# Optimization experiments

Measured on AMD Instinct MI355X. Metric: run time of the kernel, lower is better.

## Reference

```python
import jax, jax.numpy as jnp
import numpy as np

N = 32768   # points
C = 64      # channels (in == out, required by residual)
K = 16      # nsample
SP = 8      # share_planes
S = C // SP # attention channels per group
E = N * K


def _bn(t, g, b, eps=1e-5):
    # torch BatchNorm1d training-mode forward: biased batch variance
    m = t.mean(0)
    v = t.var(0)
    return (t - m) * jax.lax.rsqrt(v + eps) * g + b


def setup_inputs() -> dict:
    rng = np.random.default_rng(0)
    pos = (rng.standard_normal((N, 3)) * 10.0).astype(np.float32)
    # kNN graph (loop=True -> self is among the K nearest, distance 0), chunked
    sq = (pos ** 2).sum(1)
    nbr = np.empty((N, K), dtype=np.int64)
    chunk = 2048
    for s0 in range(0, N, chunk):
        s1 = min(s0 + chunk, N)
        d = sq[s0:s1, None] + sq[None, :] - 2.0 * (pos[s0:s1] @ pos.T)
        nbr[s0:s1] = np.argpartition(d, K - 1, axis=1)[:, :K]
    # PyG convention: edge_index[0]=source j (neighbor), edge_index[1]=target i
    edge_index = np.stack([nbr.reshape(-1),
                           np.repeat(np.arange(N, dtype=np.int64), K)])

    def lin_w(fo, fi):
        b = 1.0 / np.sqrt(fi)
        return jnp.asarray(rng.uniform(-b, b, size=(fo, fi)).astype(np.float32))

    def lin_b(fo, fi):
        b = 1.0 / np.sqrt(fi)
        return jnp.asarray(rng.uniform(-b, b, size=(fo,)).astype(np.float32))

    ones = lambda n: jnp.ones((n,), jnp.float32)
    zeros = lambda n: jnp.zeros((n,), jnp.float32)

    return {
        'pos': jnp.asarray(pos),
        'x': jnp.asarray(rng.standard_normal((N, C)).astype(np.float32)),
        'W1': lin_w(C, C),
        'Wk': lin_w(C, C), 'bk': lin_b(C, C),
        'Wq': lin_w(C, C), 'bq': lin_b(C, C),
        'Wv': lin_w(C, C), 'bv': lin_b(C, C),
        'p1_w': lin_w(3, 3), 'p1_b': lin_b(3, 3),
        'p_bn_g': ones(3), 'p_bn_b': zeros(3),
        'p2_w': lin_w(C, 3), 'p2_b': lin_b(C, 3),
        'w_bn1_g': ones(C), 'w_bn1_b': zeros(C),
        'w1_w': lin_w(S, C), 'w1_b': lin_b(S, C),
        'w_bn2_g': ones(S), 'w_bn2_b': zeros(S),
        'w2_w': lin_w(S, S), 'w2_b': lin_b(S, S),
        'W3': lin_w(C, C),
        'bn1_g': ones(C), 'bn1_b': zeros(C),
        'bn2_g': ones(C), 'bn2_b': zeros(C),
        'bn3_g': ones(C), 'bn3_b': zeros(C),
        'edge_index': jnp.asarray(edge_index),
    }


def reference(pos, x, W1, Wk, bk, Wq, bq, Wv, bv,
              p1_w, p1_b, p_bn_g, p_bn_b, p2_w, p2_b,
              w_bn1_g, w_bn1_b, w1_w, w1_b, w_bn2_g, w_bn2_b, w2_w, w2_b,
              W3, bn1_g, bn1_b, bn2_g, bn2_b, bn3_g, bn3_b, edge_index):
    x_skip = x
    h = jax.nn.relu(_bn(x @ W1.T, bn1_g, bn1_b))            # linear1 (no bias) + bn1 + relu

    # PointTransformerLayer
    k = h @ Wk.T + bk                                        # alpha_j source
    q = h @ Wq.T + bq                                        # alpha_i target
    v = h @ Wv.T + bv                                        # values
    src, dst = edge_index[0], edge_index[1]

    rel = pos[src] - pos[dst]                                # pos_j - pos_i  [E,3]
    delta = jax.nn.relu(_bn(rel @ p1_w.T + p1_b, p_bn_g, p_bn_b)) @ p2_w.T + p2_b  # [E,C]

    a = k[src] - q[dst] + delta                              # [E,C]
    a = jax.nn.relu(_bn(a, w_bn1_g, w_bn1_b)) @ w1_w.T + w1_b        # [E,S]
    a = jax.nn.relu(_bn(a, w_bn2_g, w_bn2_b)) @ w2_w.T + w2_b        # [E,S]

    # segment softmax over each target's neighborhood
    amax = jax.ops.segment_max(a, dst, num_segments=N)
    ae = jnp.exp(a - amax[dst])
    asum = jax.ops.segment_sum(ae, dst, num_segments=N)
    attn = ae / asum[dst]                                    # [E,S]

    # grouped weighted values: attn broadcast across the SP groups
    msg = (attn[:, None, :] * (v[src] + delta).reshape(E, SP, S)).reshape(E, C)
    out = jax.ops.segment_sum(msg, dst, num_segments=N)      # aggr='add' -> [N,C]

    h2 = jax.nn.relu(_bn(out, bn2_g, bn2_b))
    h3 = _bn(h2 @ W3.T, bn3_g, bn3_b)                        # linear3 (no bias) + bn3
    return jax.nn.relu(h3 + x_skip)
```

## Files before the change

### kernel.cpp

```cpp
#include <hip/hip_runtime.h>

#define NPTS 32768
#define CH 64
#define KNN 16
#define NE (NPTS*KNN)
#define EPS 1e-5f
#define NREP 32

#define G_P   0
#define G_BN1 (1*NREP*128)
#define G_W1  (2*NREP*128)
#define G_W2  (3*NREP*128)
#define G_BN2 (4*NREP*128)
#define G_BN3 (5*NREP*128)
#define STATS_FLOATS (6*NREP*128)

#define OFF_T1  (STATS_FLOATS + 512)
#define SZ_NC   (NPTS*CH)
#define OFF_K   (OFF_T1 + SZ_NC)
#define OFF_Q   (OFF_K + SZ_NC)
#define OFF_V   (OFF_Q + SZ_NC)
#define OFF_A2  (OFF_V + SZ_NC)
#define OFF_OUT (OFF_A2 + NE*8)
#define OFF_U   (OFF_OUT + SZ_NC)
#define OFF_H3  OFF_U

__device__ __forceinline__ float frelu(float x){ return fmaxf(x, 0.f); }

#define LOAD_SCSH(grp, invc, gptr, bptr, scA, shA, nch) do {                        \
    if (tid < 128) { float t_ = 0.f;                                                \
        _Pragma("unroll") for (int r_ = 0; r_ < NREP; ++r_) t_ += (grp)[r_*128+tid];\
        s_tmp[tid] = t_; }                                                          \
    __syncthreads();                                                                \
    if (tid < (nch)) { float m_ = s_tmp[tid]*(invc);                                \
        float v_ = s_tmp[64+tid]*(invc) - m_*m_;                                    \
        float s_ = (gptr)[tid]*rsqrtf(v_+EPS);                                      \
        (scA)[tid] = s_; (shA)[tid] = (bptr)[tid] - m_*s_; }                        \
    __syncthreads();                                                                \
} while(0)

__global__ __launch_bounds__(256) void k_pstats_u(
    const float* __restrict__ pos, const int* __restrict__ esrc,
    const float* __restrict__ p1w, const float* __restrict__ p1b,
    float4* __restrict__ u4, float* __restrict__ gstat)
{
    __shared__ float red[4][6];
    const int tid = threadIdx.x;
    float w[9], b3[3];
    #pragma unroll
    for (int i=0;i<9;++i) w[i]=p1w[i];
    b3[0]=p1b[0]; b3[1]=p1b[1]; b3[2]=p1b[2];
    const int e = blockIdx.x*256 + tid;
    const int sj = esrc[e]; const int d = e >> 4;
    float ax = pos[3*sj]-pos[3*d], ay = pos[3*sj+1]-pos[3*d+1], az = pos[3*sj+2]-pos[3*d+2];
    float u0 = w[0]*ax+w[1]*ay+w[2]*az+b3[0];
    float u1 = w[3]*ax+w[4]*ay+w[5]*az+b3[1];
    float u2 = w[6]*ax+w[7]*ay+w[8]*az+b3[2];
    u4[e] = make_float4(u0,u1,u2,0.f);
    float s0=u0,s1=u1,s2=u2,q0=u0*u0,q1=u1*u1,q2=u2*u2;
    #pragma unroll
    for (int m=32;m>=1;m>>=1){
        s0+=__shfl_xor(s0,m); s1+=__shfl_xor(s1,m); s2+=__shfl_xor(s2,m);
        q0+=__shfl_xor(q0,m); q1+=__shfl_xor(q1,m); q2+=__shfl_xor(q2,m);
    }
    const int wv = tid>>6;
    if ((tid&63)==0){ red[wv][0]=s0; red[wv][1]=s1; red[wv][2]=s2;
                      red[wv][3]=q0; red[wv][4]=q1; red[wv][5]=q2; }
    __syncthreads();
    float* g = gstat + (blockIdx.x & (NREP-1))*128;
    if (tid < 3)      atomicAdd(&g[tid],        red[0][tid]+red[1][tid]+red[2][tid]+red[3][tid]);
    else if (tid < 6) atomicAdd(&g[64+(tid-3)], red[0][tid]+red[1][tid]+red[2][tid]+red[3][tid]);
}

__global__ __launch_bounds__(256) void k_gemm64(
    const float* __restrict__ in, const float* __restrict__ W,
    float* __restrict__ out,
    const float* __restrict__ bnrep, const float* __restrict__ bng,
    const float* __restrict__ bnb, int applyBn,
    float* __restrict__ gstat)
{
    __shared__ float Wl[16*CH];
    __shared__ float s_tmp[128];
    __shared__ float sc[64], sh[64];
    __shared__ float red[4][32];
    const int tid = threadIdx.x;
    const int wv = tid >> 6;
    const int by = blockIdx.x >> 7;
    const int rb = blockIdx.x & 127;
    const int c0 = by*16;
    ((float4*)Wl)[tid] = ((const float4*)(W + c0*CH))[tid];
    if (applyBn) { LOAD_SCSH(bnrep, 1.f/NPTS, bng, bnb, sc, sh, 64); }
    else __syncthreads();

    const int row = rb*256 + tid;
    float xr[CH];
    {
        const float4* iv = (const float4*)(in + (size_t)row*CH);
        #pragma unroll
        for (int i=0;i<16;++i){ float4 t=iv[i];
            xr[4*i]=t.x; xr[4*i+1]=t.y; xr[4*i+2]=t.z; xr[4*i+3]=t.w; }
    }
    if (applyBn){
        #pragma unroll
        for (int i=0;i<CH;++i) xr[i] = frelu(xr[i]*sc[i]+sh[i]);
    }
    float4* ov = (float4*)(out + (size_t)row*CH + c0);
    #pragma unroll
    for (int q=0; q<4; ++q){
        float4 acc = make_float4(0,0,0,0);
        const float* w0=&Wl[(q*4+0)*CH];
        const float* w1=&Wl[(q*4+1)*CH];
        const float* w2=&Wl[(q*4+2)*CH];
        const float* w3=&Wl[(q*4+3)*CH];
        #pragma unroll
        for (int i=0;i<CH;++i){ float xv=xr[i];
            acc.x+=xv*w0[i]; acc.y+=xv*w1[i]; acc.z+=xv*w2[i]; acc.w+=xv*w3[i]; }
        ov[q]=acc;
        float4 sq = make_float4(acc.x*acc.x, acc.y*acc.y, acc.z*acc.z, acc.w*acc.w);
        #pragma unroll
        for (int m=32;m>=1;m>>=1){
            acc.x+=__shfl_xor(acc.x,m); acc.y+=__shfl_xor(acc.y,m);
            acc.z+=__shfl_xor(acc.z,m); acc.w+=__shfl_xor(acc.w,m);
            sq.x+=__shfl_xor(sq.x,m);  sq.y+=__shfl_xor(sq.y,m);
            sq.z+=__shfl_xor(sq.z,m);  sq.w+=__shfl_xor(sq.w,m);
        }
        if ((tid&63)==0){
            red[wv][q*4+0]=acc.x; red[wv][q*4+1]=acc.y; red[wv][q*4+2]=acc.z; red[wv][q*4+3]=acc.w;
            red[wv][16+q*4+0]=sq.x; red[wv][16+q*4+1]=sq.y; red[wv][16+q*4+2]=sq.z; red[wv][16+q*4+3]=sq.w;
        }
    }
    __syncthreads();
    if (tid < 32) {
        float t = red[0][tid]+red[1][tid]+red[2][tid]+red[3][tid];
        int dstc = (tid<16) ? (c0+tid) : (64 + c0 + (tid-16));
        atomicAdd(&gstat[(blockIdx.x & (NREP-1))*128 + dstc], t);
    }
}

__global__ __launch_bounds__(256) void k_kqv(
    const float* __restrict__ t1,
    const float* __restrict__ Wk, const float* __restrict__ bk,
    const float* __restrict__ Wq, const float* __restrict__ bq,
    const float* __restrict__ Wv, const float* __restrict__ bv,
    const float* __restrict__ bnrep, const float* __restrict__ bng,
    const float* __restrict__ bnb,
    float* __restrict__ kout, float* __restrict__ qout, float* __restrict__ vout)
{
    __shared__ float Wl[32*CH];
    __shared__ float bias[32];
    __shared__ float s_tmp[128];
    __shared__ float sc[64], sh[64];
    const int tid = threadIdx.x;
    const int m = blockIdx.x / 256;
    const int rem = blockIdx.x & 255;
    const int rb = rem >> 1;
    const int cbase = (rem & 1)*32;
    const float* W  = (m==0) ? Wk : (m==1 ? Wq : Wv);
    const float* bs = (m==0) ? bk : (m==1 ? bq : bv);
    float* o        = (m==0) ? kout : (m==1 ? qout : vout);
    {
        const float4* W4 = (const float4*)(W + cbase*CH);
        float4* Wl4 = (float4*)Wl;
        Wl4[tid] = W4[tid]; Wl4[256+tid] = W4[256+tid];
    }
    if (tid < 32) bias[tid] = bs[cbase+tid];
    LOAD_SCSH(bnrep, 1.f/NPTS, bng, bnb, sc, sh, 64);

    const int row = rb*256 + tid;
    float h[CH];
    {
        const float4* iv = (const float4*)(t1 + (size_t)row*CH);
        #pragma unroll
        for (int i=0;i<16;++i){ float4 t=iv[i];
            h[4*i]=t.x; h[4*i+1]=t.y; h[4*i+2]=t.z; h[4*i+3]=t.w; }
    }
    #pragma unroll
    for (int i=0;i<CH;++i) h[i] = frelu(h[i]*sc[i]+sh[i]);

    float4* ov = (float4*)(o + (size_t)row*CH + cbase);
    #pragma unroll
    for (int q=0; q<8; ++q){
        float4 acc = make_float4(bias[q*4], bias[q*4+1], bias[q*4+2], bias[q*4+3]);
        const float* w0=&Wl[(q*4+0)*CH];
        const float* w1=&Wl[(q*4+1)*CH];
        const float* w2=&Wl[(q*4+2)*CH];
        const float* w3=&Wl[(q*4+3)*CH];
        #pragma unroll
        for (int i=0;i<CH;++i){ float xv=h[i];
            acc.x+=xv*w0[i]; acc.y+=xv*w1[i]; acc.z+=xv*w2[i]; acc.w+=xv*w3[i]; }
        ov[q]=acc;
    }
}

__global__ __launch_bounds__(256) void k_edge1(
    const int* __restrict__ esrc, const float4* __restrict__ u4,
    const float* __restrict__ kbuf, const float* __restrict__ qbuf,
    const float* __restrict__ prep, const float* __restrict__ pg,
    const float* __restrict__ pb,
    const float* __restrict__ p2w, const float* __restrict__ p2b,
    float* __restrict__ gstat)
{
    __shared__ float red[4][128];
    __shared__ float s_tmp[128];
    __shared__ float scL[64], shL[64];
    const int tid = threadIdx.x;
    const int c = tid & 63, wv = tid >> 6;
    LOAD_SCSH(prep, 1.f/NE, pg, pb, scL, shL, 3);
    const float scp0=scL[0], scp1=scL[1], scp2=scL[2];
    const float shp0=shL[0], shp1=shL[1], shp2=shL[2];
    const float w0 = p2w[c*3+0], w1 = p2w[c*3+1], w2 = p2w[c*3+2], bc = p2b[c];

    const int gw = blockIdx.x*4 + wv;
    const int chunk = NE/8192;
    const int e0 = gw*chunk;
    float s=0.f, q=0.f;
    #pragma unroll 4
    for (int e = e0; e < e0+chunk; ++e) {
        int sj = esrc[e]; int d = e >> 4;
        float4 uu = u4[e];
        float r0 = frelu(uu.x*scp0+shp0);
        float r1 = frelu(uu.y*scp1+shp1);
        float r2 = frelu(uu.z*scp2+shp2);
        float a = kbuf[(size_t)sj*CH+c] - qbuf[(size_t)d*CH+c]
                + (r0*w0 + r1*w1 + r2*w2 + bc);
        s += a; q += a*a;
    }
    red[wv][c] = s; red[wv][64+c] = q;
    __syncthreads();
    if (tid < 128) {
        float t = red[0][tid]+red[1][tid]+red[2][tid]+red[3][tid];
        atomicAdd(&gstat[(blockIdx.x & (NREP-1))*128 + tid], t);
    }
}

__global__ __launch_bounds__(256) void k_edge2(
    const int* __restrict__ esrc, const float4* __restrict__ u4,
    const float* __restrict__ kbuf, const float* __restrict__ qbuf,
    const float* __restrict__ prep, const float* __restrict__ pg,
    const float* __restrict__ pb,
    const float* __restrict__ p2w, const float* __restrict__ p2b,
    const float* __restrict__ w1rep, const float* __restrict__ w1g,
    const float* __restrict__ w1bn_b,
    const float* __restrict__ w1w, const float* __restrict__ w1bias,
    float* __restrict__ a2out, float* __restrict__ gstat)
{
    __shared__ float sp2w[192], sp2b[64], sw1[512], sw1b[8];
    __shared__ float s_tmp[128];
    __shared__ float scp[64], shp[64];
    __shared__ float sc1[64], sh1[64];
    __shared__ float red[4][16];
    const int tid = threadIdx.x;
    if (tid < 192) sp2w[tid] = p2w[tid];
    if (tid < 64)  sp2b[tid] = p2b[tid];
    sw1[tid] = w1w[tid]; sw1[256+tid] = w1w[256+tid];
    if (tid < 8) sw1b[tid] = w1bias[tid];
    LOAD_SCSH(prep, 1.f/NE, pg, pb, scp, shp, 3);
    LOAD_SCSH(w1rep, 1.f/NE, w1g, w1bn_b, sc1, sh1, 64);
    const float scp0=scp[0], scp1=scp[1], scp2=scp[2];
    const float shp0=shp[0], shp1=shp[1], shp2=shp[2];

    const int e = blockIdx.x*256 + tid;
    const int sj = esrc[e]; const int d = e >> 4;
    float4 uu = u4[e];
    const float r0 = frelu(uu.x*scp0+shp0);
    const float r1 = frelu(uu.y*scp1+shp1);
    const float r2 = frelu(uu.z*scp2+shp2);
    const float4* kv = (const float4*)(kbuf + (size_t)sj*CH);
    const float4* qv = (const float4*)(qbuf + (size_t)d*CH);
    float a2a[8];
    #pragma unroll
    for (int j=0;j<8;++j) a2a[j] = sw1b[j];
    for (int cc=0; cc<16; ++cc) {
        float4 k4 = kv[cc], q4 = qv[cc];
        const int c0 = cc*4;
        float b0 = frelu((k4.x - q4.x + r0*sp2w[(c0+0)*3]+r1*sp2w[(c0+0)*3+1]+r2*sp2w[(c0+0)*3+2]+sp2b[c0+0])*sc1[c0+0]+sh1[c0+0]);
        float b1 = frelu((k4.y - q4.y + r0*sp2w[(c0+1)*3]+r1*sp2w[(c0+1)*3+1]+r2*sp2w[(c0+1)*3+2]+sp2b[c0+1])*sc1[c0+1]+sh1[c0+1]);
        float b2 = frelu((k4.z - q4.z + r0*sp2w[(c0+2)*3]+r1*sp2w[(c0+2)*3+1]+r2*sp2w[(c0+2)*3+2]+sp2b[c0+2])*sc1[c0+2]+sh1[c0+2]);
        float b3 = frelu((k4.w - q4.w + r0*sp2w[(c0+3)*3]+r1*sp2w[(c0+3)*3+1]+r2*sp2w[(c0+3)*3+2]+sp2b[c0+3])*sc1[c0+3]+sh1[c0+3]);
        #pragma unroll
        for (int j=0;j<8;++j)
            a2a[j] += b0*sw1[j*64+c0] + b1*sw1[j*64+c0+1] + b2*sw1[j*64+c0+2] + b3*sw1[j*64+c0+3];
    }
    float4* a2v = (float4*)(a2out + (size_t)e*8);
    a2v[0] = make_float4(a2a[0],a2a[1],a2a[2],a2a[3]);
    a2v[1] = make_float4(a2a[4],a2a[5],a2a[6],a2a[7]);
    float q8[8];
    #pragma unroll
    for (int j=0;j<8;++j) q8[j]=a2a[j]*a2a[j];
    #pragma unroll
    for (int m=32;m>=1;m>>=1){
        #pragma unroll
        for (int j=0;j<8;++j){ a2a[j]+=__shfl_xor(a2a[j],m); q8[j]+=__shfl_xor(q8[j],m); }
    }
    const int wv = tid>>6;
    if ((tid&63)==0){
        #pragma unroll
        for (int j=0;j<8;++j){ red[wv][j]=a2a[j]; red[wv][8+j]=q8[j]; }
    }
    __syncthreads();
    if (tid < 16) {
        float t = red[0][tid]+red[1][tid]+red[2][tid]+red[3][tid];
        int dstc = (tid<8) ? tid : (64 + tid - 8);
        atomicAdd(&gstat[(blockIdx.x & (NREP-1))*128 + dstc], t);
    }
}

__global__ __launch_bounds__(256) void k_attn(
    const int* __restrict__ esrc, const float4* __restrict__ u4,
    const float* __restrict__ vbuf, const float* __restrict__ a2buf,
    const float* __restrict__ prep, const float* __restrict__ pg,
    const float* __restrict__ pb,
    const float* __restrict__ p2w, const float* __restrict__ p2b,
    const float* __restrict__ w2rep, const float* __restrict__ w2g,
    const float* __restrict__ w2bn_b,
    const float* __restrict__ w2w, const float* __restrict__ w2bias,
    float* __restrict__ outbuf, float* __restrict__ gstat)
{
    __shared__ float sp2w[192], sp2b[64], sw2[64], sw2b[8];
    __shared__ float s_tmp[128];
    __shared__ float scp[64], shp[64];
    __shared__ float sc2[64], sh2[64];
    __shared__ float red[4][128];
    __shared__ float att[256][9];
    __shared__ float rrL[256][4];
    __shared__ int   sjL[256];
    const int tid = threadIdx.x;
    if (tid < 192) sp2w[tid] = p2w[tid];
    if (tid < 64) { sp2b[tid] = p2b[tid]; sw2[tid] = w2w[tid]; }
    if (tid < 8)  sw2b[tid] = w2bias[tid];
    LOAD_SCSH(prep, 1.f/NE, pg, pb, scp, shp, 3);
    LOAD_SCSH(w2rep, 1.f/NE, w2g, w2bn_b, sc2, sh2, 8);
    const float scp0=scp[0], scp1=scp[1], scp2=scp[2];
    const float shp0=shp[0], shp1=shp[1], shp2=shp[2];

    const int t = tid & 15;
    const int i = blockIdx.x*16 + (tid>>4);
    const int e = i*KNN + t;
    const int sj = esrc[e];
    sjL[tid] = sj;
    {
        float4 uu = u4[e];
        rrL[tid][0] = frelu(uu.x*scp0+shp0);
        rrL[tid][1] = frelu(uu.y*scp1+shp1);
        rrL[tid][2] = frelu(uu.z*scp2+shp2);
    }
    {
        const float4* a2v = (const float4*)a2buf;
        float4 aA = a2v[(size_t)e*2], aB = a2v[(size_t)e*2+1];
        float bb[8];
        bb[0]=frelu(aA.x*sc2[0]+sh2[0]); bb[1]=frelu(aA.y*sc2[1]+sh2[1]);
        bb[2]=frelu(aA.z*sc2[2]+sh2[2]); bb[3]=frelu(aA.w*sc2[3]+sh2[3]);
        bb[4]=frelu(aB.x*sc2[4]+sh2[4]); bb[5]=frelu(aB.y*sc2[5]+sh2[5]);
        bb[6]=frelu(aB.z*sc2[6]+sh2[6]); bb[7]=frelu(aB.w*sc2[7]+sh2[7]);
        #pragma unroll
        for (int s=0;s<8;++s){
            float a3 = sw2b[s];
            #pragma unroll
            for (int u=0;u<8;++u) a3 += bb[u]*sw2[s*8+u];
            float m = a3;
            #pragma unroll
            for (int msk=8;msk>=1;msk>>=1) m = fmaxf(m, __shfl_xor(m,msk));
            float p = __expf(a3-m);
            float ssm = p;
            #pragma unroll
            for (int msk=8;msk>=1;msk>>=1) ssm += __shfl_xor(ssm,msk);
            att[tid][s] = p/ssm;
        }
    }
    __syncthreads();
    const int base = (tid>>4)*16;
    const int c0 = 4*t;
    const int ho = (t&1)*4;
    const float pw00=sp2w[(c0+0)*3], pw01=sp2w[(c0+0)*3+1], pw02=sp2w[(c0+0)*3+2], pb0=sp2b[c0+0];
    const float pw10=sp2w[(c0+1)*3], pw11=sp2w[(c0+1)*3+1], pw12=sp2w[(c0+1)*3+2], pb1=sp2b[c0+1];
    const float pw20=sp2w[(c0+2)*3], pw21=sp2w[(c0+2)*3+1], pw22=sp2w[(c0+2)*3+2], pb2=sp2b[c0+2];
    const float pw30=sp2w[(c0+3)*3], pw31=sp2w[(c0+3)*3+1], pw32=sp2w[(c0+3)*3+2], pb3=sp2b[c0+3];
    float4 res = make_float4(0,0,0,0);
    #pragma unroll 4
    for (int n=0; n<16; ++n){
        const int sjn = sjL[base+n];
        float4 v4 = ((const float4*)(vbuf + (size_t)sjn*CH))[t];
        const float rr0 = rrL[base+n][0], rr1 = rrL[base+n][1], rr2 = rrL[base+n][2];
        const float a0 = att[base+n][ho+0], a1 = att[base+n][ho+1];
        const float a2_ = att[base+n][ho+2], a3 = att[base+n][ho+3];
        res.x += a0*(v4.x + rr0*pw00+rr1*pw01+rr2*pw02+pb0);
        res.y += a1*(v4.y + rr0*pw10+rr1*pw11+rr2*pw12+pb1);
        res.z += a2_*(v4.z + rr0*pw20+rr1*pw21+rr2*pw22+pb2);
        res.w += a3*(v4.w + rr0*pw30+rr1*pw31+rr2*pw32+pb3);
    }
    ((float4*)outbuf)[(size_t)i*16 + t] = res;

    float4 sq = make_float4(res.x*res.x, res.y*res.y, res.z*res.z, res.w*res.w);
    #pragma unroll
    for (int msk=32;msk>=16;msk>>=1){
        res.x+=__shfl_xor(res.x,msk); res.y+=__shfl_xor(res.y,msk);
        res.z+=__shfl_xor(res.z,msk); res.w+=__shfl_xor(res.w,msk);
        sq.x+=__shfl_xor(sq.x,msk);  sq.y+=__shfl_xor(sq.y,msk);
        sq.z+=__shfl_xor(sq.z,msk);  sq.w+=__shfl_xor(sq.w,msk);
    }
    const int wv = tid>>6;
    if ((tid&63) < 16){
        red[wv][t*4+0]=res.x; red[wv][t*4+1]=res.y; red[wv][t*4+2]=res.z; red[wv][t*4+3]=res.w;
        red[wv][64+t*4+0]=sq.x; red[wv][64+t*4+1]=sq.y; red[wv][64+t*4+2]=sq.z; red[wv][64+t*4+3]=sq.w;
    }
    __syncthreads();
    if (tid < 128) {
        float tt = red[0][tid]+red[1][tid]+red[2][tid]+red[3][tid];
        atomicAdd(&gstat[(blockIdx.x & (NREP-1))*128 + tid], tt);
    }
}

__global__ __launch_bounds__(256) void k_final(
    const float* __restrict__ h3, const float* __restrict__ x,
    const float* __restrict__ bnrep, const float* __restrict__ g,
    const float* __restrict__ b, float* __restrict__ out)
{
    __shared__ float s_tmp[128];
    __shared__ float sc[64], sh[64];
    const int tid = threadIdx.x;
    LOAD_SCSH(bnrep, 1.f/NPTS, g, b, sc, sh, 64);
    const int gi = blockIdx.x*256 + tid;
    const int c0 = (gi & 15)*4;
    float4 h = ((const float4*)h3)[gi];
    float4 xv = ((const float4*)x)[gi];
    float4 o;
    o.x = fmaxf(h.x*sc[c0+0]+sh[c0+0]+xv.x, 0.f);
    o.y = fmaxf(h.y*sc[c0+1]+sh[c0+1]+xv.y, 0.f);
    o.z = fmaxf(h.z*sc[c0+2]+sh[c0+2]+xv.z, 0.f);
    o.w = fmaxf(h.w*sc[c0+3]+sh[c0+3]+xv.w, 0.f);
    ((float4*)out)[gi] = o;
}

extern "C" void kernel_launch(void* const* d_in, const int* in_sizes, int n_in,
                              void* d_out, int out_size, void* d_ws, size_t ws_size,
                              hipStream_t stream) {
    (void)in_sizes; (void)n_in; (void)out_size; (void)ws_size;
    const float* pos   = (const float*)d_in[0];
    const float* x     = (const float*)d_in[1];
    const float* W1    = (const float*)d_in[2];
    const float* Wk    = (const float*)d_in[3];
    const float* bk    = (const float*)d_in[4];
    const float* Wq    = (const float*)d_in[5];
    const float* bq    = (const float*)d_in[6];
    const float* Wv    = (const float*)d_in[7];
    const float* bv    = (const float*)d_in[8];
    const float* p1w   = (const float*)d_in[9];
    const float* p1b   = (const float*)d_in[10];
    const float* pg    = (const float*)d_in[11];
    const float* pb    = (const float*)d_in[12];
    const float* p2w   = (const float*)d_in[13];
    const float* p2b   = (const float*)d_in[14];
    const float* w1g   = (const float*)d_in[15];
    const float* w1bb  = (const float*)d_in[16];
    const float* w1w   = (const float*)d_in[17];
    const float* w1bias= (const float*)d_in[18];
    const float* w2g   = (const float*)d_in[19];
    const float* w2bb  = (const float*)d_in[20];
    const float* w2w   = (const float*)d_in[21];
    const float* w2bias= (const float*)d_in[22];
    const float* W3    = (const float*)d_in[23];
    const float* bn1g  = (const float*)d_in[24];
    const float* bn1b  = (const float*)d_in[25];
    const float* bn2g  = (const float*)d_in[26];
    const float* bn2b  = (const float*)d_in[27];
    const float* bn3g  = (const float*)d_in[28];
    const float* bn3b  = (const float*)d_in[29];
    const int*   ei    = (const int*)d_in[30];
    float* ws  = (float*)d_ws;
    float* out = (float*)d_out;

    hipMemsetAsync(ws, 0, STATS_FLOATS*sizeof(float), stream);

    k_pstats_u<<<2048, 256, 0, stream>>>(pos, ei, p1w, p1b,
        (float4*)(ws+OFF_U), ws+G_P);
    k_gemm64<<<512, 256, 0, stream>>>(x, W1, ws+OFF_T1,
        nullptr, nullptr, nullptr, 0, ws+G_BN1);
    k_kqv<<<768, 256, 0, stream>>>(ws+OFF_T1, Wk, bk, Wq, bq, Wv, bv,
        ws+G_BN1, bn1g, bn1b, ws+OFF_K, ws+OFF_Q, ws+OFF_V);
    k_edge1<<<2048, 256, 0, stream>>>(ei, (const float4*)(ws+OFF_U),
        ws+OFF_K, ws+OFF_Q, ws+G_P, pg, pb, p2w, p2b, ws+G_W1);
    k_edge2<<<2048, 256, 0, stream>>>(ei, (const float4*)(ws+OFF_U),
        ws+OFF_K, ws+OFF_Q, ws+G_P, pg, pb, p2w, p2b,
        ws+G_W1, w1g, w1bb, w1w, w1bias, ws+OFF_A2, ws+G_W2);
    k_attn<<<2048, 256, 0, stream>>>(ei, (const float4*)(ws+OFF_U),
        ws+OFF_V, ws+OFF_A2, ws+G_P, pg, pb, p2w, p2b,
        ws+G_W2, w2g, w2bb, w2w, w2bias, ws+OFF_OUT, ws+G_BN2);
    k_gemm64<<<512, 256, 0, stream>>>(ws+OFF_OUT, W3, ws+OFF_H3,
        ws+G_BN2, bn2g, bn2b, 1, ws+G_BN3);
    k_final<<<2048, 256, 0, stream>>>(ws+OFF_H3, x, ws+G_BN3, bn3g, bn3b, out);
}
```

Baseline: 311.5 us.

## Precompute BN scale/shift in tiny finalize kernels, drop per-block LDS staging

Moves BatchNorm statistic finalization (summing the replicated partial sums and computing scale/shift) out of every block into small dedicated k_fin launches. Consumer kernels now read the finished scale/shift and the weights directly from global memory through the scalar/constant cache, with no LDS staging or __syncthreads prologue. The attention buffer is repacked to 8-wide rows so it can be read and written as float4. This trades redundant per-block reductions and barriers for five extra kernel launches and uniform global loads in the inner loops.

```diff
diff --git a/kernel.cpp b/kernel.cpp
--- a/kernel.cpp
+++ b/kernel.cpp
@@ -15,7 +15,14 @@
 #define G_BN3 (5*NREP*128)
 #define STATS_FLOATS (6*NREP*128)
 
-#define OFF_T1  (STATS_FLOATS + 512)
+#define F_P   (STATS_FLOATS + 0*128)
+#define F_BN1 (STATS_FLOATS + 1*128)
+#define F_W1  (STATS_FLOATS + 2*128)
+#define F_W2  (STATS_FLOATS + 3*128)
+#define F_BN2 (STATS_FLOATS + 4*128)
+#define F_BN3 (STATS_FLOATS + 5*128)
+
+#define OFF_T1  (STATS_FLOATS + 1024)
 #define SZ_NC   (NPTS*CH)
 #define OFF_K   (OFF_T1 + SZ_NC)
 #define OFF_Q   (OFF_K + SZ_NC)
@@ -27,17 +34,31 @@
 
 __device__ __forceinline__ float frelu(float x){ return fmaxf(x, 0.f); }
 
-#define LOAD_SCSH(grp, invc, gptr, bptr, scA, shA, nch) do {                        \
-    if (tid < 128) { float t_ = 0.f;                                                \
-        _Pragma("unroll") for (int r_ = 0; r_ < NREP; ++r_) t_ += (grp)[r_*128+tid];\
-        s_tmp[tid] = t_; }                                                          \
-    __syncthreads();                                                                \
-    if (tid < (nch)) { float m_ = s_tmp[tid]*(invc);                                \
-        float v_ = s_tmp[64+tid]*(invc) - m_*m_;                                    \
-        float s_ = (gptr)[tid]*rsqrtf(v_+EPS);                                      \
-        (scA)[tid] = s_; (shA)[tid] = (bptr)[tid] - m_*s_; }                        \
-    __syncthreads();                                                                \
-} while(0)
+__global__ __launch_bounds__(128) void k_fin(
+    const float* __restrict__ gA, float invA, const float* __restrict__ gmA,
+    const float* __restrict__ btA, float* __restrict__ outA, int nchA,
+    const float* __restrict__ gB, float invB, const float* __restrict__ gmB,
+    const float* __restrict__ btB, float* __restrict__ outB, int nchB)
+{
+    __shared__ float s_tmp[128];
+    const int tid = threadIdx.x;
+    const float* g; float inv; const float* gm; const float* bt; float* o; int nch;
+    if (blockIdx.x == 0) { g=gA; inv=invA; gm=gmA; bt=btA; o=outA; nch=nchA; }
+    else { if (!outB) return; g=gB; inv=invB; gm=gmB; bt=btB; o=outB; nch=nchB; }
+    float t = 0.f;
+    #pragma unroll
+    for (int r=0;r<NREP;++r) t += g[r*128+tid];
+    s_tmp[tid] = t;
+    __syncthreads();
+    if (tid < 64) {
+        if (tid < nch) {
+            float m = s_tmp[tid]*inv;
+            float v = s_tmp[64+tid]*inv - m*m;
+            float s = gm[tid]*rsqrtf(v+EPS);
+            o[tid] = s; o[64+tid] = bt[tid] - m*s;
+        } else { o[tid]=0.f; o[64+tid]=0.f; }
+    }
+}
 
 __global__ __launch_bounds__(256) void k_pstats_u(
     const float* __restrict__ pos, const int* __restrict__ esrc,
@@ -46,16 +67,14 @@
 {
     __shared__ float red[4][6];
     const int tid = threadIdx.x;
-    float w[9], b3[3];
-    #pragma unroll
-    for (int i=0;i<9;++i) w[i]=p1w[i];
-    b3[0]=p1b[0]; b3[1]=p1b[1]; b3[2]=p1b[2];
+    const float w0=p1w[0],w1=p1w[1],w2=p1w[2],w3=p1w[3],w4=p1w[4],w5=p1w[5],w6=p1w[6],w7=p1w[7],w8=p1w[8];
+    const float b0=p1b[0],b1=p1b[1],b2=p1b[2];
     const int e = blockIdx.x*256 + tid;
     const int sj = esrc[e]; const int d = e >> 4;
     float ax = pos[3*sj]-pos[3*d], ay = pos[3*sj+1]-pos[3*d+1], az = pos[3*sj+2]-pos[3*d+2];
-    float u0 = w[0]*ax+w[1]*ay+w[2]*az+b3[0];
-    float u1 = w[3]*ax+w[4]*ay+w[5]*az+b3[1];
-    float u2 = w[6]*ax+w[7]*ay+w[8]*az+b3[2];
+    float u0 = w0*ax+w1*ay+w2*az+b0;
+    float u1 = w3*ax+w4*ay+w5*az+b1;
+    float u2 = w6*ax+w7*ay+w8*az+b2;
     u4[e] = make_float4(u0,u1,u2,0.f);
     float s0=u0,s1=u1,s2=u2,q0=u0*u0,q1=u1*u1,q2=u2*u2;
     #pragma unroll
@@ -75,23 +94,15 @@
 __global__ __launch_bounds__(256) void k_gemm64(
     const float* __restrict__ in, const float* __restrict__ W,
     float* __restrict__ out,
-    const float* __restrict__ bnrep, const float* __restrict__ bng,
-    const float* __restrict__ bnb, int applyBn,
+    const float* __restrict__ fbn, int applyBn,
     float* __restrict__ gstat)
 {
-    __shared__ float Wl[16*CH];
-    __shared__ float s_tmp[128];
-    __shared__ float sc[64], sh[64];
     __shared__ float red[4][32];
     const int tid = threadIdx.x;
     const int wv = tid >> 6;
     const int by = blockIdx.x >> 7;
     const int rb = blockIdx.x & 127;
     const int c0 = by*16;
-    ((float4*)Wl)[tid] = ((const float4*)(W + c0*CH))[tid];
-    if (applyBn) { LOAD_SCSH(bnrep, 1.f/NPTS, bng, bnb, sc, sh, 64); }
-    else __syncthreads();
-
     const int row = rb*256 + tid;
     float xr[CH];
     {
@@ -102,19 +113,19 @@
     }
     if (applyBn){
         #pragma unroll
-        for (int i=0;i<CH;++i) xr[i] = frelu(xr[i]*sc[i]+sh[i]);
+        for (int i=0;i<CH;++i) xr[i] = frelu(xr[i]*fbn[i]+fbn[64+i]);
     }
     float4* ov = (float4*)(out + (size_t)row*CH + c0);
     #pragma unroll
     for (int q=0; q<4; ++q){
         float4 acc = make_float4(0,0,0,0);
-        const float* w0=&Wl[(q*4+0)*CH];
-        const float* w1=&Wl[(q*4+1)*CH];
-        const float* w2=&Wl[(q*4+2)*CH];
-        const float* w3=&Wl[(q*4+3)*CH];
+        const float* wr0 = W + (size_t)(c0+q*4+0)*CH;
+        const float* wr1 = W + (size_t)(c0+q*4+1)*CH;
+        const float* wr2 = W + (size_t)(c0+q*4+2)*CH;
+        const float* wr3 = W + (size_t)(c0+q*4+3)*CH;
         #pragma unroll
         for (int i=0;i<CH;++i){ float xv=xr[i];
-            acc.x+=xv*w0[i]; acc.y+=xv*w1[i]; acc.z+=xv*w2[i]; acc.w+=xv*w3[i]; }
+            acc.x+=xv*wr0[i]; acc.y+=xv*wr1[i]; acc.z+=xv*wr2[i]; acc.w+=xv*wr3[i]; }
         ov[q]=acc;
         float4 sq = make_float4(acc.x*acc.x, acc.y*acc.y, acc.z*acc.z, acc.w*acc.w);
         #pragma unroll
@@ -142,14 +153,9 @@
     const float* __restrict__ Wk, const float* __restrict__ bk,
     const float* __restrict__ Wq, const float* __restrict__ bq,
     const float* __restrict__ Wv, const float* __restrict__ bv,
-    const float* __restrict__ bnrep, const float* __restrict__ bng,
-    const float* __restrict__ bnb,
+    const float* __restrict__ fbn,
     float* __restrict__ kout, float* __restrict__ qout, float* __restrict__ vout)
 {
-    __shared__ float Wl[32*CH];
-    __shared__ float bias[32];
-    __shared__ float s_tmp[128];
-    __shared__ float sc[64], sh[64];
     const int tid = threadIdx.x;
     const int m = blockIdx.x / 256;
     const int rem = blockIdx.x & 255;
@@ -158,13 +164,6 @@
     const float* W  = (m==0) ? Wk : (m==1 ? Wq : Wv);
     const float* bs = (m==0) ? bk : (m==1 ? bq : bv);
     float* o        = (m==0) ? kout : (m==1 ? qout : vout);
-    {
-        const float4* W4 = (const float4*)(W + cbase*CH);
-        float4* Wl4 = (float4*)Wl;
-        Wl4[tid] = W4[tid]; Wl4[256+tid] = W4[256+tid];
-    }
-    if (tid < 32) bias[tid] = bs[cbase+tid];
-    LOAD_SCSH(bnrep, 1.f/NPTS, bng, bnb, sc, sh, 64);
 
     const int row = rb*256 + tid;
     float h[CH];
@@ -175,19 +174,19 @@
             h[4*i]=t.x; h[4*i+1]=t.y; h[4*i+2]=t.z; h[4*i+3]=t.w; }
     }
     #pragma unroll
-    for (int i=0;i<CH;++i) h[i] = frelu(h[i]*sc[i]+sh[i]);
+    for (int i=0;i<CH;++i) h[i] = frelu(h[i]*fbn[i]+fbn[64+i]);
 
     float4* ov = (float4*)(o + (size_t)row*CH + cbase);
     #pragma unroll
     for (int q=0; q<8; ++q){
-        float4 acc = make_float4(bias[q*4], bias[q*4+1], bias[q*4+2], bias[q*4+3]);
-        const float* w0=&Wl[(q*4+0)*CH];
-        const float* w1=&Wl[(q*4+1)*CH];
-        const float* w2=&Wl[(q*4+2)*CH];
-        const float* w3=&Wl[(q*4+3)*CH];
+        float4 acc = make_float4(bs[cbase+q*4], bs[cbase+q*4+1], bs[cbase+q*4+2], bs[cbase+q*4+3]);
+        const float* wr0 = W + (size_t)(cbase+q*4+0)*CH;
+        const float* wr1 = W + (size_t)(cbase+q*4+1)*CH;
+        const float* wr2 = W + (size_t)(cbase+q*4+2)*CH;
+        const float* wr3 = W + (size_t)(cbase+q*4+3)*CH;
         #pragma unroll
         for (int i=0;i<CH;++i){ float xv=h[i];
-            acc.x+=xv*w0[i]; acc.y+=xv*w1[i]; acc.z+=xv*w2[i]; acc.w+=xv*w3[i]; }
+            acc.x+=xv*wr0[i]; acc.y+=xv*wr1[i]; acc.z+=xv*wr2[i]; acc.w+=xv*wr3[i]; }
         ov[q]=acc;
     }
 }
@@ -195,19 +194,15 @@
 __global__ __launch_bounds__(256) void k_edge1(
     const int* __restrict__ esrc, const float4* __restrict__ u4,
     const float* __restrict__ kbuf, const float* __restrict__ qbuf,
-    const float* __restrict__ prep, const float* __restrict__ pg,
-    const float* __restrict__ pb,
+    const float* __restrict__ fP,
     const float* __restrict__ p2w, const float* __restrict__ p2b,
     float* __restrict__ gstat)
 {
     __shared__ float red[4][128];
-    __shared__ float s_tmp[128];
-    __shared__ float scL[64], shL[64];
     const int tid = threadIdx.x;
     const int c = tid & 63, wv = tid >> 6;
-    LOAD_SCSH(prep, 1.f/NE, pg, pb, scL, shL, 3);
-    const float scp0=scL[0], scp1=scL[1], scp2=scL[2];
-    const float shp0=shL[0], shp1=shL[1], shp2=shL[2];
+    const float scp0=fP[0], scp1=fP[1], scp2=fP[2];
+    const float shp0=fP[64], shp1=fP[65], shp2=fP[66];
     const float w0 = p2w[c*3+0], w1 = p2w[c*3+1], w2 = p2w[c*3+2], bc = p2b[c];
 
     const int gw = blockIdx.x*4 + wv;
@@ -236,28 +231,16 @@
 __global__ __launch_bounds__(256) void k_edge2(
     const int* __restrict__ esrc, const float4* __restrict__ u4,
     const float* __restrict__ kbuf, const float* __restrict__ qbuf,
-    const float* __restrict__ prep, const float* __restrict__ pg,
-    const float* __restrict__ pb,
+    const float* __restrict__ fP,
     const float* __restrict__ p2w, const float* __restrict__ p2b,
-    const float* __restrict__ w1rep, const float* __restrict__ w1g,
-    const float* __restrict__ w1bn_b,
+    const float* __restrict__ fW1,
     const float* __restrict__ w1w, const float* __restrict__ w1bias,
     float* __restrict__ a2out, float* __restrict__ gstat)
 {
-    __shared__ float sp2w[192], sp2b[64], sw1[512], sw1b[8];
-    __shared__ float s_tmp[128];
-    __shared__ float scp[64], shp[64];
-    __shared__ float sc1[64], sh1[64];
     __shared__ float red[4][16];
     const int tid = threadIdx.x;
-    if (tid < 192) sp2w[tid] = p2w[tid];
-    if (tid < 64)  sp2b[tid] = p2b[tid];
-    sw1[tid] = w1w[tid]; sw1[256+tid] = w1w[256+tid];
-    if (tid < 8) sw1b[tid] = w1bias[tid];
-    LOAD_SCSH(prep, 1.f/NE, pg, pb, scp, shp, 3);
-    LOAD_SCSH(w1rep, 1.f/NE, w1g, w1bn_b, sc1, sh1, 64);
-    const float scp0=scp[0], scp1=scp[1], scp2=scp[2];
-    const float shp0=shp[0], shp1=shp[1], shp2=shp[2];
+    const float scp0=fP[0], scp1=fP[1], scp2=fP[2];
+    const float shp0=fP[64], shp1=fP[65], shp2=fP[66];
 
     const int e = blockIdx.x*256 + tid;
     const int sj = esrc[e]; const int d = e >> 4;
@@ -269,17 +252,18 @@
     const float4* qv = (const float4*)(qbuf + (size_t)d*CH);
     float a2a[8];
     #pragma unroll
-    for (int j=0;j<8;++j) a2a[j] = sw1b[j];
+    for (int j=0;j<8;++j) a2a[j] = w1bias[j];
+    #pragma unroll
     for (int cc=0; cc<16; ++cc) {
         float4 k4 = kv[cc], q4 = qv[cc];
         const int c0 = cc*4;
-        float b0 = frelu((k4.x - q4.x + r0*sp2w[(c0+0)*3]+r1*sp2w[(c0+0)*3+1]+r2*sp2w[(c0+0)*3+2]+sp2b[c0+0])*sc1[c0+0]+sh1[c0+0]);
-        float b1 = frelu((k4.y - q4.y + r0*sp2w[(c0+1)*3]+r1*sp2w[(c0+1)*3+1]+r2*sp2w[(c0+1)*3+2]+sp2b[c0+1])*sc1[c0+1]+sh1[c0+1]);
-        float b2 = frelu((k4.z - q4.z + r0*sp2w[(c0+2)*3]+r1*sp2w[(c0+2)*3+1]+r2*sp2w[(c0+2)*3+2]+sp2b[c0+2])*sc1[c0+2]+sh1[c0+2]);
-        float b3 = frelu((k4.w - q4.w + r0*sp2w[(c0+3)*3]+r1*sp2w[(c0+3)*3+1]+r2*sp2w[(c0+3)*3+2]+sp2b[c0+3])*sc1[c0+3]+sh1[c0+3]);
+        float b0 = frelu((k4.x - q4.x + r0*p2w[(c0+0)*3]+r1*p2w[(c0+0)*3+1]+r2*p2w[(c0+0)*3+2]+p2b[c0+0])*fW1[c0+0]+fW1[64+c0+0]);
+        float b1 = frelu((k4.y - q4.y + r0*p2w[(c0+1)*3]+r1*p2w[(c0+1)*3+1]+r2*p2w[(c0+1)*3+2]+p2b[c0+1])*fW1[c0+1]+fW1[64+c0+1]);
+        float b2 = frelu((k4.z - q4.z + r0*p2w[(c0+2)*3]+r1*p2w[(c0+2)*3+1]+r2*p2w[(c0+2)*3+2]+p2b[c0+2])*fW1[c0+2]+fW1[64+c0+2]);
+        float b3 = frelu((k4.w - q4.w + r0*p2w[(c0+3)*3]+r1*p2w[(c0+3)*3+1]+r2*p2w[(c0+3)*3+2]+p2b[c0+3])*fW1[c0+3]+fW1[64+c0+3]);
         #pragma unroll
         for (int j=0;j<8;++j)
-            a2a[j] += b0*sw1[j*64+c0] + b1*sw1[j*64+c0+1] + b2*sw1[j*64+c0+2] + b3*sw1[j*64+c0+3];
+            a2a[j] += b0*w1w[j*64+c0] + b1*w1w[j*64+c0+1] + b2*w1w[j*64+c0+2] + b3*w1w[j*64+c0+3];
     }
     float4* a2v = (float4*)(a2out + (size_t)e*8);
     a2v[0] = make_float4(a2a[0],a2a[1],a2a[2],a2a[3]);
@@ -308,30 +292,19 @@
 __global__ __launch_bounds__(256) void k_attn(
     const int* __restrict__ esrc, const float4* __restrict__ u4,
     const float* __restrict__ vbuf, const float* __restrict__ a2buf,
-    const float* __restrict__ prep, const float* __restrict__ pg,
-    const float* __restrict__ pb,
+    const float* __restrict__ fP,
     const float* __restrict__ p2w, const float* __restrict__ p2b,
-    const float* __restrict__ w2rep, const float* __restrict__ w2g,
-    const float* __restrict__ w2bn_b,
+    const float* __restrict__ fW2,
     const float* __restrict__ w2w, const float* __restrict__ w2bias,
     float* __restrict__ outbuf, float* __restrict__ gstat)
 {
-    __shared__ float sp2w[192], sp2b[64], sw2[64], sw2b[8];
-    __shared__ float s_tmp[128];
-    __shared__ float scp[64], shp[64];
-    __shared__ float sc2[64], sh2[64];
     __shared__ float red[4][128];
-    __shared__ float att[256][9];
+    __shared__ float att[256][8];
     __shared__ float rrL[256][4];
     __shared__ int   sjL[256];
     const int tid = threadIdx.x;
-    if (tid < 192) sp2w[tid] = p2w[tid];
-    if (tid < 64) { sp2b[tid] = p2b[tid]; sw2[tid] = w2w[tid]; }
-    if (tid < 8)  sw2b[tid] = w2bias[tid];
-    LOAD_SCSH(prep, 1.f/NE, pg, pb, scp, shp, 3);
-    LOAD_SCSH(w2rep, 1.f/NE, w2g, w2bn_b, sc2, sh2, 8);
-    const float scp0=scp[0], scp1=scp[1], scp2=scp[2];
-    const float shp0=shp[0], shp1=shp[1], shp2=shp[2];
+    const float scp0=fP[0], scp1=fP[1], scp2=fP[2];
+    const float shp0=fP[64], shp1=fP[65], shp2=fP[66];
 
     const int t = tid & 15;
     const int i = blockIdx.x*16 + (tid>>4);
@@ -348,15 +321,16 @@
         const float4* a2v = (const float4*)a2buf;
         float4 aA = a2v[(size_t)e*2], aB = a2v[(size_t)e*2+1];
         float bb[8];
-        bb[0]=frelu(aA.x*sc2[0]+sh2[0]); bb[1]=frelu(aA.y*sc2[1]+sh2[1]);
-        bb[2]=frelu(aA.z*sc2[2]+sh2[2]); bb[3]=frelu(aA.w*sc2[3]+sh2[3]);
-        bb[4]=frelu(aB.x*sc2[4]+sh2[4]); bb[5]=frelu(aB.y*sc2[5]+sh2[5]);
-        bb[6]=frelu(aB.z*sc2[6]+sh2[6]); bb[7]=frelu(aB.w*sc2[7]+sh2[7]);
+        bb[0]=frelu(aA.x*fW2[0]+fW2[64]); bb[1]=frelu(aA.y*fW2[1]+fW2[65]);
+        bb[2]=frelu(aA.z*fW2[2]+fW2[66]); bb[3]=frelu(aA.w*fW2[3]+fW2[67]);
+        bb[4]=frelu(aB.x*fW2[4]+fW2[68]); bb[5]=frelu(aB.y*fW2[5]+fW2[69]);
+        bb[6]=frelu(aB.z*fW2[6]+fW2[70]); bb[7]=frelu(aB.w*fW2[7]+fW2[71]);
+        float at[8];
         #pragma unroll
         for (int s=0;s<8;++s){
-            float a3 = sw2b[s];
+            float a3 = w2bias[s];
             #pragma unroll
-            for (int u=0;u<8;++u) a3 += bb[u]*sw2[s*8+u];
+            for (int u=0;u<8;++u) a3 += bb[u]*w2w[s*8+u];
             float m = a3;
             #pragma unroll
             for (int msk=8;msk>=1;msk>>=1) m = fmaxf(m, __shfl_xor(m,msk));
@@ -364,29 +338,31 @@
             float ssm = p;
             #pragma unroll
             for (int msk=8;msk>=1;msk>>=1) ssm += __shfl_xor(ssm,msk);
-            att[tid][s] = p/ssm;
+            at[s] = p/ssm;
         }
+        ((float4*)att[tid])[0] = make_float4(at[0],at[1],at[2],at[3]);
+        ((float4*)att[tid])[1] = make_float4(at[4],at[5],at[6],at[7]);
     }
     __syncthreads();
     const int base = (tid>>4)*16;
     const int c0 = 4*t;
-    const int ho = (t&1)*4;
-    const float pw00=sp2w[(c0+0)*3], pw01=sp2w[(c0+0)*3+1], pw02=sp2w[(c0+0)*3+2], pb0=sp2b[c0+0];
-    const float pw10=sp2w[(c0+1)*3], pw11=sp2w[(c0+1)*3+1], pw12=sp2w[(c0+1)*3+2], pb1=sp2b[c0+1];
-    const float pw20=sp2w[(c0+2)*3], pw21=sp2w[(c0+2)*3+1], pw22=sp2w[(c0+2)*3+2], pb2=sp2b[c0+2];
-    const float pw30=sp2w[(c0+3)*3], pw31=sp2w[(c0+3)*3+1], pw32=sp2w[(c0+3)*3+2], pb3=sp2b[c0+3];
+    const int ho = (t&1);
+    float pw[12], pbv[4];
+    #pragma unroll
+    for (int k2=0;k2<12;++k2) pw[k2] = p2w[c0*3+k2];
+    #pragma unroll
+    for (int k2=0;k2<4;++k2)  pbv[k2] = p2b[c0+k2];
     float4 res = make_float4(0,0,0,0);
     #pragma unroll 4
     for (int n=0; n<16; ++n){
         const int sjn = sjL[base+n];
         float4 v4 = ((const float4*)(vbuf + (size_t)sjn*CH))[t];
         const float rr0 = rrL[base+n][0], rr1 = rrL[base+n][1], rr2 = rrL[base+n][2];
-        const float a0 = att[base+n][ho+0], a1 = att[base+n][ho+1];
-        const float a2_ = att[base+n][ho+2], a3 = att[base+n][ho+3];
-        res.x += a0*(v4.x + rr0*pw00+rr1*pw01+rr2*pw02+pb0);
-        res.y += a1*(v4.y + rr0*pw10+rr1*pw11+rr2*pw12+pb1);
-        res.z += a2_*(v4.z + rr0*pw20+rr1*pw21+rr2*pw22+pb2);
-        res.w += a3*(v4.w + rr0*pw30+rr1*pw31+rr2*pw32+pb3);
+        float4 a4 = ((const float4*)att[base+n])[ho];
+        res.x += a4.x*(v4.x + rr0*pw[0]+rr1*pw[1]+rr2*pw[2]+pbv[0]);
+        res.y += a4.y*(v4.y + rr0*pw[3]+rr1*pw[4]+rr2*pw[5]+pbv[1]);
+        res.z += a4.z*(v4.z + rr0*pw[6]+rr1*pw[7]+rr2*pw[8]+pbv[2]);
+        res.w += a4.w*(v4.w + rr0*pw[9]+rr1*pw[10]+rr2*pw[11]+pbv[3]);
     }
     ((float4*)outbuf)[(size_t)i*16 + t] = res;
 
@@ -412,22 +388,20 @@
 
 __global__ __launch_bounds__(256) void k_final(
     const float* __restrict__ h3, const float* __restrict__ x,
-    const float* __restrict__ bnrep, const float* __restrict__ g,
-    const float* __restrict__ b, float* __restrict__ out)
-{
-    __shared__ float s_tmp[128];
-    __shared__ float sc[64], sh[64];
-    const int tid = threadIdx.x;
-    LOAD_SCSH(bnrep, 1.f/NPTS, g, b, sc, sh, 64);
+    const float* __restrict__ fbn, float* __restrict__ out)
+{
+    const int tid = threadIdx.x;
     const int gi = blockIdx.x*256 + tid;
     const int c0 = (gi & 15)*4;
+    float sc0=fbn[c0],sc1=fbn[c0+1],sc2=fbn[c0+2],sc3=fbn[c0+3];
+    float sh0=fbn[64+c0],sh1=fbn[64+c0+1],sh2=fbn[64+c0+2],sh3=fbn[64+c0+3];
     float4 h = ((const float4*)h3)[gi];
     float4 xv = ((const float4*)x)[gi];
     float4 o;
-    o.x = fmaxf(h.x*sc[c0+0]+sh[c0+0]+xv.x, 0.f);
-    o.y = fmaxf(h.y*sc[c0+1]+sh[c0+1]+xv.y, 0.f);
-    o.z = fmaxf(h.z*sc[c0+2]+sh[c0+2]+xv.z, 0.f);
-    o.w = fmaxf(h.w*sc[c0+3]+sh[c0+3]+xv.w, 0.f);
+    o.x = fmaxf(h.x*sc0+sh0+xv.x, 0.f);
+    o.y = fmaxf(h.y*sc1+sh1+xv.y, 0.f);
+    o.z = fmaxf(h.z*sc2+sh2+xv.z, 0.f);
+    o.w = fmaxf(h.w*sc3+sh3+xv.w, 0.f);
     ((float4*)out)[gi] = o;
 }
 
@@ -473,19 +447,28 @@
 
     k_pstats_u<<<2048, 256, 0, stream>>>(pos, ei, p1w, p1b,
         (float4*)(ws+OFF_U), ws+G_P);
-    k_gemm64<<<512, 256, 0, stream>>>(x, W1, ws+OFF_T1,
-        nullptr, nullptr, nullptr, 0, ws+G_BN1);
+    k_gemm64<<<512, 256, 0, stream>>>(x, W1, ws+OFF_T1, nullptr, 0, ws+G_BN1);
+    k_fin<<<2, 128, 0, stream>>>(ws+G_P, 1.f/NE, pg, pb, ws+F_P, 3,
+                                 ws+G_BN1, 1.f/NPTS, bn1g, bn1b, ws+F_BN1, 64);
     k_kqv<<<768, 256, 0, stream>>>(ws+OFF_T1, Wk, bk, Wq, bq, Wv, bv,
-        ws+G_BN1, bn1g, bn1b, ws+OFF_K, ws+OFF_Q, ws+OFF_V);
+        ws+F_BN1, ws+OFF_K, ws+OFF_Q, ws+OFF_V);
     k_edge1<<<2048, 256, 0, stream>>>(ei, (const float4*)(ws+OFF_U),
-        ws+OFF_K, ws+OFF_Q, ws+G_P, pg, pb, p2w, p2b, ws+G_W1);
+        ws+OFF_K, ws+OFF_Q, ws+F_P, p2w, p2b, ws+G_W1);
+    k_fin<<<1, 128, 0, stream>>>(ws+G_W1, 1.f/NE, w1g, w1bb, ws+F_W1, 64,
+                                 nullptr, 0.f, nullptr, nullptr, nullptr, 0);
     k_edge2<<<2048, 256, 0, stream>>>(ei, (const float4*)(ws+OFF_U),
-        ws+OFF_K, ws+OFF_Q, ws+G_P, pg, pb, p2w, p2b,
-        ws+G_W1, w1g, w1bb, w1w, w1bias, ws+OFF_A2, ws+G_W2);
+        ws+OFF_K, ws+OFF_Q, ws+F_P, p2w, p2b,
+        ws+F_W1, w1w, w1bias, ws+OFF_A2, ws+G_W2);
+    k_fin<<<1, 128, 0, stream>>>(ws+G_W2, 1.f/NE, w2g, w2bb, ws+F_W2, 8,
+                                 nullptr, 0.f, nullptr, nullptr, nullptr, 0);
     k_attn<<<2048, 256, 0, stream>>>(ei, (const float4*)(ws+OFF_U),
-        ws+OFF_V, ws+OFF_A2, ws+G_P, pg, pb, p2w, p2b,
-        ws+G_W2, w2g, w2bb, w2w, w2bias, ws+OFF_OUT, ws+G_BN2);
+        ws+OFF_V, ws+OFF_A2, ws+F_P, p2w, p2b,
+        ws+F_W2, w2w, w2bias, ws+OFF_OUT, ws+G_BN2);
+    k_fin<<<1, 128, 0, stream>>>(ws+G_BN2, 1.f/NPTS, bn2g, bn2b, ws+F_BN2, 64,
+                                 nullptr, 0.f, nullptr, nullptr, nullptr, 0);
     k_gemm64<<<512, 256, 0, stream>>>(ws+OFF_OUT, W3, ws+OFF_H3,
-        ws+G_BN2, bn2g, bn2b, 1, ws+G_BN3);
-    k_final<<<2048, 256, 0, stream>>>(ws+OFF_H3, x, ws+G_BN3, bn3g, bn3b, out);
-}
+        ws+F_BN2, 1, ws+G_BN3);
+    k_fin<<<1, 128, 0, stream>>>(ws+G_BN3, 1.f/NPTS, bn3g, bn3b, ws+F_BN3, 64,
+                                 nullptr, 0.f, nullptr, nullptr, nullptr, 0);
+    k_final<<<2048, 256, 0, stream>>>(ws+OFF_H3, x, ws+F_BN3, out);
+}
```

Result: slower. 325.7 us (+4.5%).
